# Kernel optimization log

Hardware: AMD Instinct MI355X
Metric: run time of the kernel (lower is better)

The kernel has to match this reference:

```python
import jax, jax.numpy as jnp
import numpy as np

W_BITS = 8       # default precision = max(precisions)
MIN_PREC = 4     # min(precisions)
GROUP_SIZE = 128


def make_new_byte_indices(total_bytes: int) -> np.ndarray:
    # Replicates make_new_byte_indices_torch. Note: in the torch code,
    # argsort(argsort(new_idx)) == new_idx (it is a permutation), so the
    # "unpermute" is a gather with new_idx itself.
    bytes_per_thread = 4
    threads_per_warp = 32
    bytes_per_warp = threads_per_warp * bytes_per_thread  # 128
    full = total_bytes // bytes_per_warp * bytes_per_warp
    rem = total_bytes - full
    parts = []
    if full > 0:
        bi = np.arange(full)
        warp_offsets = (bi // bytes_per_warp) * bytes_per_warp
        thread_indices = bi % threads_per_warp
        byte_off = ((bi % bytes_per_warp) // threads_per_warp) ^ 3
        parts.append(warp_offsets + thread_indices * bytes_per_thread + byte_off)
    if rem > 0:
        ri = np.arange(rem)
        adj = rem // bytes_per_thread
        if adj > 0:
            warp_offsets = (ri // bytes_per_warp) * bytes_per_warp
            thread_indices = ri % adj
            byte_off = (ri // adj) ^ 3
            parts.append(warp_offsets + thread_indices * 4 + byte_off + full)
        else:
            parts.append(np.arange(full, full + rem))
    return np.concatenate(parts).astype(np.int64)


def dequant(qweight, scale, zero, w_bits=W_BITS):
    _, N, in_chunks = qweight.shape
    total_bytes = in_chunks * 4
    in_features = in_chunks * 32
    q = qweight[:w_bits]
    # little-endian byte view of int32 (matches torch .view(torch.uint8))
    b = jnp.stack([(q >> (8 * k)) & 0xFF for k in range(4)], axis=-1)
    b = b.reshape(w_bits, N, total_bytes)  # int32 values in [0,255]
    idx = jnp.asarray(make_new_byte_indices(total_bytes))
    b = b[:, :, idx]
    # unpack bits, MSB first within each byte
    bits = jnp.stack([(b >> i) & 1 for i in reversed(range(8))], axis=-1)
    bits = bits.reshape(w_bits, N, in_features)  # [w_bits, N, in_features]
    plane_w = jnp.asarray([1 << (w_bits - 1 - k) for k in range(w_bits)], dtype=jnp.int32)
    qw = jnp.einsum('b,bni->ni', plane_w, bits)  # int32 in [0, 2^w_bits-1]
    weight_f = qw.astype(jnp.float32)
    bit_err = w_bits - MIN_PREC
    zero = zero * (2.0 ** bit_err)
    scale_pc = jnp.repeat(scale, GROUP_SIZE, axis=1)[:, :in_features]
    zero_pc = jnp.repeat(zero, GROUP_SIZE, axis=1)[:, :in_features]
    return scale_pc * (weight_f - zero_pc)  # [N, in_features]


def setup_inputs() -> dict:
    key = jax.random.key(0)
    kx, kq, ks, kz, kb = jax.random.split(key, 5)
    B, S, IN, OUT, G = 4, 2048, 4096, 4096, GROUP_SIZE
    x = jax.random.normal(kx, (B, S, IN), dtype=jnp.float32)
    qweight = jax.random.randint(kq, (8, OUT, IN // 32), 0, 2147483647, dtype=jnp.int32)
    scale = jax.random.uniform(ks, (OUT, IN // G), dtype=jnp.float32) * 0.01 + 1e-4
    zero = jax.random.uniform(kz, (OUT, IN // G), dtype=jnp.float32) * 8.0
    bias = jax.random.normal(kb, (OUT,), dtype=jnp.float32)
    return {"x": x, "qweight": qweight, "scale": scale, "zero": zero, "bias": bias}


def reference(x, qweight, scale, zero, bias):
    weight = dequant(qweight, scale, zero, W_BITS)  # [out, in]
    return jnp.matmul(x, weight.T) + bias
```

## Files before the change

kernel.cpp:

```cpp
#include <hip/hip_runtime.h>
#include <hip/hip_bf16.h>
#include <stdint.h>

typedef __attribute__((ext_vector_type(8))) short short8;
typedef __attribute__((ext_vector_type(4))) float f32x4;

#define M_DIM 8192
#define N_DIM 4096
#define K_DIM 4096
#define BM 256
#define BN 256
#define BK 64

static __device__ __forceinline__ unsigned short f32_to_bf16(float f) {
  union { float f; unsigned int u; } v; v.f = f;
  unsigned int u = v.u;
  u += 0x7fffu + ((u >> 16) & 1u);
  return (unsigned short)(u >> 16);
}

__global__ void prep_kernel(const float* __restrict__ x,
                            unsigned short* __restrict__ xb,
                            const int* __restrict__ qw,
                            const float* __restrict__ scale,
                            const float* __restrict__ zero,
                            unsigned short* __restrict__ W) {
  if (blockIdx.x < 16384) {
    size_t i = ((size_t)blockIdx.x * blockDim.x + threadIdx.x) * 8;
    float4 v0 = *reinterpret_cast<const float4*>(x + i);
    float4 v1 = *reinterpret_cast<const float4*>(x + i + 4);
    short8 o;
    o[0] = (short)f32_to_bf16(v0.x);
    o[1] = (short)f32_to_bf16(v0.y);
    o[2] = (short)f32_to_bf16(v0.z);
    o[3] = (short)f32_to_bf16(v0.w);
    o[4] = (short)f32_to_bf16(v1.x);
    o[5] = (short)f32_to_bf16(v1.y);
    o[6] = (short)f32_to_bf16(v1.z);
    o[7] = (short)f32_to_bf16(v1.w);
    *reinterpret_cast<short8*>(xb + i) = o;
  } else {
    int idx = (blockIdx.x - 16384) * blockDim.x + threadIdx.x;
    int n = idx >> 7;
    int c = idx & 127;
    unsigned int w[8];
#pragma unroll
    for (int k = 0; k < 8; ++k)
      w[k] = (unsigned int)qw[(size_t)k * (N_DIM * 128) + idx];
    int wp = c >> 5, t = c & 31;
#pragma unroll
    for (int s = 0; s < 4; ++s) {
      int r = s ^ 3;
      unsigned int by[8];
#pragma unroll
      for (int k = 0; k < 8; ++k) by[k] = (w[k] >> (8 * r)) & 0xffu;
      int ibase = wp * 1024 + s * 256 + t * 8;
      int g = ibase >> 7;
      float sc = scale[n * 32 + g];
      float zp = zero[n * 32 + g] * 16.0f;
      short8 o;
#pragma unroll
      for (int u = 0; u < 8; ++u) {
        unsigned int q = 0;
#pragma unroll
        for (int k = 0; k < 8; ++k)
          q |= ((by[k] >> (7 - u)) & 1u) << (7 - k);
        o[u] = (short)f32_to_bf16(sc * ((float)q - zp));
      }
      *reinterpret_cast<short8*>(&W[(size_t)n * K_DIM + ibase]) = o;
    }
  }
}


#define VMCNT2 asm volatile("s_waitcnt vmcnt(2)" ::: "memory")
#define VMCNT0 asm volatile("s_waitcnt vmcnt(0)" ::: "memory")
#define NOOP ((void)0)
#define SB0 __builtin_amdgcn_sched_barrier(0)

#define STG(G, GROWB, KT, LDSC) do {                                           \
  const unsigned short* sb_ = (G) + ((size_t)(GROWB) * K_DIM + (KT) * 64);     \
  __builtin_amdgcn_global_load_lds(                                            \
      (const __attribute__((address_space(1))) void*)(sb_ + s_off0),           \
      (__attribute__((address_space(3))) void*)(smem + (LDSC) + wslot),        \
      16, 0, 0);                                                               \
  __builtin_amdgcn_global_load_lds(                                            \
      (const __attribute__((address_space(1))) void*)(sb_ + s_off1),           \
      (__attribute__((address_space(3))) void*)(smem + (LDSC) + 8192 + wslot), \
      16, 0, 0);                                                               \
} while (0)
#define STG_A(BUF, H, KT) STG(Ag, m0 + (H)*128, (KT), ((BUF)*2 + (H)) * 16384)
#define STG_B(BUF, H, KT) STG(Bg, n0 + (H)*128, (KT), 65536 + ((BUF)*2 + (H)) * 16384)

#define LA_H(BUF, QM, KK, M0) do {                                             \
  _Pragma("unroll") for (int mf_ = M0; mf_ < (M0) + 2; ++mf_)                  \
    a_[mf_][KK] = *(const short8*)(smem + ((KK) ? a_off1 : a_off0) +           \
        (((BUF)*2 + (QM)) * 16384 + mf_ * 2048));                              \
} while (0)
#define LB(BUF, QN, KK) do {                                                   \
  _Pragma("unroll") for (int nf_ = 0; nf_ < 2; ++nf_)                          \
    b_[nf_][KK] = *(const short8*)(smem + ((KK) ? b_off1 : b_off0) +           \
        (((BUF)*2 + (QN)) * 16384 + nf_ * 2048));                              \
} while (0)

#define MFMA_Q(QM, QN, KK, M0)                                                 \
  _Pragma("unroll") for (int mf_ = M0; mf_ < (M0) + 2; ++mf_)                  \
    _Pragma("unroll") for (int nf_ = 0; nf_ < 2; ++nf_)                        \
      acc[QM][QN][mf_][nf_] = __builtin_amdgcn_mfma_f32_16x16x32_bf16(         \
          a_[mf_][KK], b_[nf_][KK], acc[QM][QN][mf_][nf_], 0, 0, 0)

#define REGION(QM, QN, R1, R2, R3, R4, STAGE, WAITV) do {                      \
  __builtin_amdgcn_s_barrier();                                                \
  WAITV;                                                                       \
  SB0;                                                                         \
  __builtin_amdgcn_s_setprio(1);                                               \
  STAGE;                                                                       \
  SB0;                                                                         \
  MFMA_Q(QM, QN, 0, 0); SB0; R1; SB0;                                          \
  MFMA_Q(QM, QN, 0, 2); SB0; R2; SB0;                                          \
  MFMA_Q(QM, QN, 1, 0); SB0; R3; SB0;                                          \
  MFMA_Q(QM, QN, 1, 2); SB0; R4; SB0;                                          \
  __builtin_amdgcn_s_setprio(0);                                               \
} while (0)

__global__ __launch_bounds__(512, 2) void gemm_kernel(
    const unsigned short* __restrict__ Ag,
    const unsigned short* __restrict__ Bg,
    const float* __restrict__ bias,
    float* __restrict__ C) {
  __shared__ __align__(16) char smem[131072];

  int bid = blockIdx.x;
  int cpx = gridDim.x >> 3;
  int swz = (bid & 7) * cpx + (bid >> 3);
  int tm = swz >> 4;
  int tn = swz & 15;
  int m0 = tm * BM, n0 = tn * BN;

  int tid = threadIdx.x;
  int lane = tid & 63;
  int wid = tid >> 6;
  int wr = wid >> 2, wc = wid & 3;

  const int xorv = (lane & 7) << 4;
  const int hi4 = (lane >> 4) << 4;
  const int wrbase = wr * 64 + (lane & 15);
  const int wcbase = wc * 32 + (lane & 15);
  const int a_off0 = (wrbase << 7) + (hi4 ^ xorv);
  const int a_off1 = (wrbase << 7) + ((64 | hi4) ^ xorv);
  const int b_off0 = 65536 + (wcbase << 7) + (hi4 ^ xorv);
  const int b_off1 = 65536 + (wcbase << 7) + ((64 | hi4) ^ xorv);
  const int wslot = (tid >> 6) << 10;
  const int s_lr0 = tid >> 3, s_lr1 = 64 + (tid >> 3);
  const int s_off0 = s_lr0 * K_DIM + (((tid & 7) ^ (s_lr0 & 7)) << 3);
  const int s_off1 = s_lr1 * K_DIM + (((tid & 7) ^ (s_lr1 & 7)) << 3);

  short8 a_[4][2], b_[2][2];
  f32x4 acc[2][2][4][2];
#pragma unroll
  for (int i = 0; i < 2; ++i)
#pragma unroll
    for (int j = 0; j < 2; ++j)
#pragma unroll
      for (int mf = 0; mf < 4; ++mf)
#pragma unroll
        for (int nf = 0; nf < 2; ++nf) acc[i][j][mf][nf] = (f32x4){0.f, 0.f, 0.f, 0.f};

  STG_B(0, 0, 0); STG_A(0, 0, 0); STG_B(0, 1, 0); STG_A(0, 1, 0);
  STG_A(1, 0, 1);
  VMCNT2;
  __builtin_amdgcn_s_barrier();
  LA_H(0, 0, 0, 0); LA_H(0, 0, 0, 2); LB(0, 0, 0);
  LA_H(0, 0, 1, 0); LA_H(0, 0, 1, 2); LB(0, 0, 1);

  for (int t = 0; t < 31; ++t) {
    const int kt1 = 2 * t + 1;
    REGION(0, 0, NOOP,            LB(0,1,0),                  NOOP,            LB(0,1,1),                  STG_B(1,0,kt1),   VMCNT2);
    REGION(0, 1, LA_H(0,1,0,0),   LA_H(0,1,0,2),              LA_H(0,1,1,0),   LA_H(0,1,1,2),              STG_B(1,1,kt1),   VMCNT2);
    REGION(1, 1, NOOP,            LB(0,0,0),                  NOOP,            LB(0,0,1),                  STG_A(1,1,kt1),   VMCNT2);
    REGION(1, 0, LA_H(1,0,0,0),   LA_H(1,0,0,2); LB(1,0,0),   LA_H(1,0,1,0),   LA_H(1,0,1,2); LB(1,0,1),   STG_B(0,0,kt1+1), VMCNT2);
    REGION(0, 0, NOOP,            LB(1,1,0),                  NOOP,            LB(1,1,1),                  STG_A(0,0,kt1+1), VMCNT2);
    REGION(0, 1, LA_H(1,1,0,0),   LA_H(1,1,0,2),              LA_H(1,1,1,0),   LA_H(1,1,1,2),              STG_B(0,1,kt1+1), VMCNT2);
    REGION(1, 1, NOOP,            LB(1,0,0),                  NOOP,            LB(1,0,1),                  STG_A(0,1,kt1+1), VMCNT2);
    REGION(1, 0, LA_H(0,0,0,0),   LA_H(0,0,0,2); LB(0,0,0),   LA_H(0,0,1,0),   LA_H(0,0,1,2); LB(0,0,1),   STG_A(1,0,kt1+2), VMCNT2);
  }
  REGION(0, 0, NOOP,            LB(0,1,0),                  NOOP,            LB(0,1,1),                  STG_B(1,0,63), VMCNT2);
  REGION(0, 1, LA_H(0,1,0,0),   LA_H(0,1,0,2),              LA_H(0,1,1,0),   LA_H(0,1,1,2),              STG_B(1,1,63), VMCNT2);
  REGION(1, 1, NOOP,            LB(0,0,0),                  NOOP,            LB(0,0,1),                  STG_A(1,1,63), VMCNT2);
  REGION(1, 0, LA_H(1,0,0,0),   LA_H(1,0,0,2); LB(1,0,0),   LA_H(1,0,1,0),   LA_H(1,0,1,2); LB(1,0,1),   NOOP,          VMCNT2);
  REGION(0, 0, NOOP,            LB(1,1,0),                  NOOP,            LB(1,1,1),                  NOOP,          VMCNT0);
  REGION(0, 1, LA_H(1,1,0,0),   LA_H(1,1,0,2),              LA_H(1,1,1,0),   LA_H(1,1,1,2),              NOOP,          NOOP);
  REGION(1, 1, NOOP,            LB(1,0,0),                  NOOP,            LB(1,0,1),                  NOOP,          NOOP);
  REGION(1, 0, NOOP,            NOOP,                       NOOP,            NOOP,                       NOOP,          NOOP);

#pragma unroll
  for (int qn = 0; qn < 2; ++qn)
#pragma unroll
    for (int nf = 0; nf < 2; ++nf) {
      int gcol = n0 + qn * 128 + wc * 32 + nf * 16 + (lane & 15);
      float bv = bias[gcol];
#pragma unroll
      for (int qm = 0; qm < 2; ++qm)
#pragma unroll
        for (int mf = 0; mf < 4; ++mf) {
          int grow = m0 + qm * 128 + wr * 64 + mf * 16 + ((lane >> 4) << 2);
          f32x4 v = acc[qm][qn][mf][nf];
#pragma unroll
          for (int j = 0; j < 4; ++j)
            C[(size_t)(grow + j) * N_DIM + gcol] = v[j] + bv;
        }
    }
}

extern "C" void kernel_launch(void* const* d_in, const int* in_sizes, int n_in,
                              void* d_out, int out_size, void* d_ws, size_t ws_size,
                              hipStream_t stream) {
  const float* x       = (const float*)d_in[0];
  const int*   qweight = (const int*)d_in[1];
  const float* scale   = (const float*)d_in[2];
  const float* zero    = (const float*)d_in[3];
  const float* bias    = (const float*)d_in[4];
  float* out = (float*)d_out;

  unsigned short* Xb = (unsigned short*)d_ws;
  unsigned short* Wb = Xb + (size_t)M_DIM * K_DIM;

  prep_kernel<<<16384 + 2048, 256, 0, stream>>>(x, Xb, qweight, scale, zero, Wb);
  gemm_kernel<<<(M_DIM / BM) * (N_DIM / BN), 512, 0, stream>>>(Xb, Wb, bias, out);
}
```

Baseline: 263.6 us.

## Switch GEMM inner loop from 16x16x32 to 32x32x16 bf16 MFMA

Replaces the 16x16x32 MFMA tiling with 32x32x16 MFMA instructions. This changes the per-wave fragment layout, the LDS read offsets and swizzle, the accumulator shape and the epilogue store mapping. The larger MFMA shape means fewer LDS fragment reads per flop and fewer instructions per tile. In exchange the interleaving of reads and MFMAs within each region is coarser, and the epilogue writes rows with a different lane pattern.

```diff
diff --git a/kernel.cpp b/kernel.cpp
--- a/kernel.cpp
+++ b/kernel.cpp
@@ -4,6 +4,7 @@
 
 typedef __attribute__((ext_vector_type(8))) short short8;
 typedef __attribute__((ext_vector_type(4))) float f32x4;
+typedef __attribute__((ext_vector_type(16))) float f32x16;
 
 #define M_DIM 8192
 #define N_DIM 4096
@@ -92,34 +93,35 @@
 #define STG_A(BUF, H, KT) STG(Ag, m0 + (H)*128, (KT), ((BUF)*2 + (H)) * 16384)
 #define STG_B(BUF, H, KT) STG(Bg, n0 + (H)*128, (KT), 65536 + ((BUF)*2 + (H)) * 16384)
 
-#define LA_H(BUF, QM, KK, M0) do {                                             \
-  _Pragma("unroll") for (int mf_ = M0; mf_ < (M0) + 2; ++mf_)                  \
-    a_[mf_][KK] = *(const short8*)(smem + ((KK) ? a_off1 : a_off0) +           \
-        (((BUF)*2 + (QM)) * 16384 + mf_ * 2048));                              \
-} while (0)
-#define LB(BUF, QN, KK) do {                                                   \
-  _Pragma("unroll") for (int nf_ = 0; nf_ < 2; ++nf_)                          \
-    b_[nf_][KK] = *(const short8*)(smem + ((KK) ? b_off1 : b_off0) +           \
-        (((BUF)*2 + (QN)) * 16384 + nf_ * 2048));                              \
-} while (0)
-
-#define MFMA_Q(QM, QN, KK, M0)                                                 \
-  _Pragma("unroll") for (int mf_ = M0; mf_ < (M0) + 2; ++mf_)                  \
-    _Pragma("unroll") for (int nf_ = 0; nf_ < 2; ++nf_)                        \
-      acc[QM][QN][mf_][nf_] = __builtin_amdgcn_mfma_f32_16x16x32_bf16(         \
-          a_[mf_][KK], b_[nf_][KK], acc[QM][QN][mf_][nf_], 0, 0, 0)
-
-#define REGION(QM, QN, R1, R2, R3, R4, STAGE, WAITV) do {                      \
+#define LA_H(BUF, QM, J0) do {                                                 \
+  _Pragma("unroll") for (int j_ = J0; j_ < (J0) + 2; ++j_)                     \
+    _Pragma("unroll") for (int mf_ = 0; mf_ < 2; ++mf_)                        \
+      am_[mf_][j_] = *(const short8*)(smem + av[j_] +                          \
+          (((BUF)*2 + (QM)) * 16384 + mf_ * 4096));                            \
+} while (0)
+#define LB_H(BUF, QN, J0) do {                                                 \
+  _Pragma("unroll") for (int j_ = J0; j_ < (J0) + 2; ++j_)                     \
+    bn_[j_] = *(const short8*)(smem + bv[j_] + (((BUF)*2 + (QN)) * 16384));    \
+} while (0)
+
+#define MFMA_H(QM, QN, J0)                                                     \
+  _Pragma("unroll") for (int j_ = J0; j_ < (J0) + 2; ++j_)                     \
+    _Pragma("unroll") for (int mf_ = 0; mf_ < 2; ++mf_)                        \
+      acc[QM][QN][mf_] = __builtin_amdgcn_mfma_f32_32x32x16_bf16(              \
+          am_[mf_][j_], bn_[j_], acc[QM][QN][mf_], 0, 0, 0)
+
+#define REGION(QM, QN, RD0, RD1, STAGE, WAITV) do {                            \
   __builtin_amdgcn_s_barrier();                                                \
   WAITV;                                                                       \
   SB0;                                                                         \
   __builtin_amdgcn_s_setprio(1);                                               \
   STAGE;                                                                       \
+  MFMA_H(QM, QN, 0);                                                           \
+  RD0;                                                                         \
   SB0;                                                                         \
-  MFMA_Q(QM, QN, 0, 0); SB0; R1; SB0;                                          \
-  MFMA_Q(QM, QN, 0, 2); SB0; R2; SB0;                                          \
-  MFMA_Q(QM, QN, 1, 0); SB0; R3; SB0;                                          \
-  MFMA_Q(QM, QN, 1, 2); SB0; R4; SB0;                                          \
+  MFMA_H(QM, QN, 2);                                                           \
+  RD1;                                                                         \
+  SB0;                                                                         \
   __builtin_amdgcn_s_setprio(0);                                               \
 } while (0)
 
@@ -142,74 +144,76 @@
   int wid = tid >> 6;
   int wr = wid >> 2, wc = wid & 3;
 
-  const int xorv = (lane & 7) << 4;
-  const int hi4 = (lane >> 4) << 4;
-  const int wrbase = wr * 64 + (lane & 15);
-  const int wcbase = wc * 32 + (lane & 15);
-  const int a_off0 = (wrbase << 7) + (hi4 ^ xorv);
-  const int a_off1 = (wrbase << 7) + ((64 | hi4) ^ xorv);
-  const int b_off0 = 65536 + (wcbase << 7) + (hi4 ^ xorv);
-  const int b_off1 = 65536 + (wcbase << 7) + ((64 | hi4) ^ xorv);
+  const int l31 = lane & 31;
+  const int khalf16 = (lane >> 5) << 4;
+  const int arow = wr * 64 + l31;
+  const int bcol = wc * 32 + l31;
+  const int axor = (arow & 7) << 4;
+  const int bxor = (bcol & 7) << 4;
+  int av[4], bv[4];
+#pragma unroll
+  for (int j = 0; j < 4; ++j) {
+    av[j] = (arow << 7) + ((j * 32 + khalf16) ^ axor);
+    bv[j] = 65536 + (bcol << 7) + ((j * 32 + khalf16) ^ bxor);
+  }
   const int wslot = (tid >> 6) << 10;
   const int s_lr0 = tid >> 3, s_lr1 = 64 + (tid >> 3);
   const int s_off0 = s_lr0 * K_DIM + (((tid & 7) ^ (s_lr0 & 7)) << 3);
   const int s_off1 = s_lr1 * K_DIM + (((tid & 7) ^ (s_lr1 & 7)) << 3);
 
-  short8 a_[4][2], b_[2][2];
-  f32x4 acc[2][2][4][2];
+  short8 am_[2][4], bn_[4];
+  f32x16 acc[2][2][2];
 #pragma unroll
   for (int i = 0; i < 2; ++i)
 #pragma unroll
     for (int j = 0; j < 2; ++j)
 #pragma unroll
-      for (int mf = 0; mf < 4; ++mf)
-#pragma unroll
-        for (int nf = 0; nf < 2; ++nf) acc[i][j][mf][nf] = (f32x4){0.f, 0.f, 0.f, 0.f};
+      for (int m = 0; m < 2; ++m)
+#pragma unroll
+        for (int e = 0; e < 16; ++e) acc[i][j][m][e] = 0.f;
 
   STG_B(0, 0, 0); STG_A(0, 0, 0); STG_B(0, 1, 0); STG_A(0, 1, 0);
   STG_A(1, 0, 1);
   VMCNT2;
   __builtin_amdgcn_s_barrier();
-  LA_H(0, 0, 0, 0); LA_H(0, 0, 0, 2); LB(0, 0, 0);
-  LA_H(0, 0, 1, 0); LA_H(0, 0, 1, 2); LB(0, 0, 1);
+  LA_H(0, 0, 0); LA_H(0, 0, 2); LB_H(0, 0, 0); LB_H(0, 0, 2);
 
   for (int t = 0; t < 31; ++t) {
     const int kt1 = 2 * t + 1;
-    REGION(0, 0, NOOP,            LB(0,1,0),                  NOOP,            LB(0,1,1),                  STG_B(1,0,kt1),   VMCNT2);
-    REGION(0, 1, LA_H(0,1,0,0),   LA_H(0,1,0,2),              LA_H(0,1,1,0),   LA_H(0,1,1,2),              STG_B(1,1,kt1),   VMCNT2);
-    REGION(1, 1, NOOP,            LB(0,0,0),                  NOOP,            LB(0,0,1),                  STG_A(1,1,kt1),   VMCNT2);
-    REGION(1, 0, LA_H(1,0,0,0),   LA_H(1,0,0,2); LB(1,0,0),   LA_H(1,0,1,0),   LA_H(1,0,1,2); LB(1,0,1),   STG_B(0,0,kt1+1), VMCNT2);
-    REGION(0, 0, NOOP,            LB(1,1,0),                  NOOP,            LB(1,1,1),                  STG_A(0,0,kt1+1), VMCNT2);
-    REGION(0, 1, LA_H(1,1,0,0),   LA_H(1,1,0,2),              LA_H(1,1,1,0),   LA_H(1,1,1,2),              STG_B(0,1,kt1+1), VMCNT2);
-    REGION(1, 1, NOOP,            LB(1,0,0),                  NOOP,            LB(1,0,1),                  STG_A(0,1,kt1+1), VMCNT2);
-    REGION(1, 0, LA_H(0,0,0,0),   LA_H(0,0,0,2); LB(0,0,0),   LA_H(0,0,1,0),   LA_H(0,0,1,2); LB(0,0,1),   STG_A(1,0,kt1+2), VMCNT2);
-  }
-  REGION(0, 0, NOOP,            LB(0,1,0),                  NOOP,            LB(0,1,1),                  STG_B(1,0,63), VMCNT2);
-  REGION(0, 1, LA_H(0,1,0,0),   LA_H(0,1,0,2),              LA_H(0,1,1,0),   LA_H(0,1,1,2),              STG_B(1,1,63), VMCNT2);
-  REGION(1, 1, NOOP,            LB(0,0,0),                  NOOP,            LB(0,0,1),                  STG_A(1,1,63), VMCNT2);
-  REGION(1, 0, LA_H(1,0,0,0),   LA_H(1,0,0,2); LB(1,0,0),   LA_H(1,0,1,0),   LA_H(1,0,1,2); LB(1,0,1),   NOOP,          VMCNT2);
-  REGION(0, 0, NOOP,            LB(1,1,0),                  NOOP,            LB(1,1,1),                  NOOP,          VMCNT0);
-  REGION(0, 1, LA_H(1,1,0,0),   LA_H(1,1,0,2),              LA_H(1,1,1,0),   LA_H(1,1,1,2),              NOOP,          NOOP);
-  REGION(1, 1, NOOP,            LB(1,0,0),                  NOOP,            LB(1,0,1),                  NOOP,          NOOP);
-  REGION(1, 0, NOOP,            NOOP,                       NOOP,            NOOP,                       NOOP,          NOOP);
-
-#pragma unroll
-  for (int qn = 0; qn < 2; ++qn)
-#pragma unroll
-    for (int nf = 0; nf < 2; ++nf) {
-      int gcol = n0 + qn * 128 + wc * 32 + nf * 16 + (lane & 15);
-      float bv = bias[gcol];
-#pragma unroll
-      for (int qm = 0; qm < 2; ++qm)
-#pragma unroll
-        for (int mf = 0; mf < 4; ++mf) {
-          int grow = m0 + qm * 128 + wr * 64 + mf * 16 + ((lane >> 4) << 2);
-          f32x4 v = acc[qm][qn][mf][nf];
-#pragma unroll
-          for (int j = 0; j < 4; ++j)
-            C[(size_t)(grow + j) * N_DIM + gcol] = v[j] + bv;
+    REGION(0, 0, LB_H(0,1,0),              LB_H(0,1,2),              STG_B(1,0,kt1),   VMCNT2);
+    REGION(0, 1, LA_H(0,1,0),              LA_H(0,1,2),              STG_B(1,1,kt1),   VMCNT2);
+    REGION(1, 1, LB_H(0,0,0),              LB_H(0,0,2),              STG_A(1,1,kt1),   VMCNT2);
+    REGION(1, 0, LA_H(1,0,0); LB_H(1,0,0), LA_H(1,0,2); LB_H(1,0,2), STG_B(0,0,kt1+1), VMCNT2);
+    REGION(0, 0, LB_H(1,1,0),              LB_H(1,1,2),              STG_A(0,0,kt1+1), VMCNT2);
+    REGION(0, 1, LA_H(1,1,0),              LA_H(1,1,2),              STG_B(0,1,kt1+1), VMCNT2);
+    REGION(1, 1, LB_H(1,0,0),              LB_H(1,0,2),              STG_A(0,1,kt1+1), VMCNT2);
+    REGION(1, 0, LA_H(0,0,0); LB_H(0,0,0), LA_H(0,0,2); LB_H(0,0,2), STG_A(1,0,kt1+2), VMCNT2);
+  }
+  REGION(0, 0, LB_H(0,1,0),              LB_H(0,1,2),              STG_B(1,0,63), VMCNT2);
+  REGION(0, 1, LA_H(0,1,0),              LA_H(0,1,2),              STG_B(1,1,63), VMCNT2);
+  REGION(1, 1, LB_H(0,0,0),              LB_H(0,0,2),              STG_A(1,1,63), VMCNT2);
+  REGION(1, 0, LA_H(1,0,0); LB_H(1,0,0), LA_H(1,0,2); LB_H(1,0,2), NOOP,          VMCNT2);
+  REGION(0, 0, LB_H(1,1,0),              LB_H(1,1,2),              NOOP,          VMCNT0);
+  REGION(0, 1, LA_H(1,1,0),              LA_H(1,1,2),              NOOP,          NOOP);
+  REGION(1, 1, LB_H(1,0,0),              LB_H(1,0,2),              NOOP,          NOOP);
+  REGION(1, 0, NOOP,                     NOOP,                     NOOP,          NOOP);
+
+#pragma unroll
+  for (int qn = 0; qn < 2; ++qn) {
+    int gcol = n0 + qn * 128 + wc * 32 + l31;
+    float bvf = bias[gcol];
+#pragma unroll
+    for (int qm = 0; qm < 2; ++qm)
+#pragma unroll
+      for (int m = 0; m < 2; ++m) {
+        int growb = m0 + qm * 128 + wr * 64 + m * 32 + ((lane >> 5) << 2);
+#pragma unroll
+        for (int reg = 0; reg < 16; ++reg) {
+          int grow = growb + (reg & 3) + 8 * (reg >> 2);
+          C[(size_t)grow * N_DIM + gcol] = acc[qm][qn][m][reg] + bvf;
         }
-    }
+      }
+  }
 }
 
 extern "C" void kernel_launch(void* const* d_in, const int* in_sizes, int n_in,
```

Measured after the change: 282.8 us. 1.07x slower.
